# Optimization experiments

Measured on AMD Instinct MI355X. Metric: run time of the kernel, lower is better.

Reference implementation:

```python
import jax, jax.numpy as jnp
import numpy as np

BS, QLEN, DIM, NH = 2, 2048, 1024, 16
HD = DIM // NH


def setup_inputs() -> dict:
    key = jax.random.key(0)
    ks = jax.random.split(key, 6)
    std = 0.02
    return {
        "x": jax.random.normal(ks[0], (BS, QLEN, DIM), dtype=jnp.float32),
        "mask": jnp.ones((BS, QLEN), dtype=jnp.float32),
        "Wq": jax.random.normal(ks[1], (DIM, DIM), dtype=jnp.float32) * std,
        "bq": jnp.zeros((DIM,), dtype=jnp.float32),
        "Wk": jax.random.normal(ks[2], (DIM, DIM), dtype=jnp.float32) * std,
        "bk": jnp.zeros((DIM,), dtype=jnp.float32),
        "Wv": jax.random.normal(ks[3], (DIM, DIM), dtype=jnp.float32) * std,
        "bv": jnp.zeros((DIM,), dtype=jnp.float32),
        "Wo": jax.random.normal(ks[4], (DIM, DIM), dtype=jnp.float32) * std,
        "bo": jnp.zeros((DIM,), dtype=jnp.float32),
    }


def reference(x, mask, Wq, bq, Wk, bk, Wv, bv, Wo, bo):
    bs, qlen, dim = x.shape
    # project and split heads: [bs, nh, len, hd]
    def split_heads(t):
        return t.reshape(bs, -1, NH, HD).transpose(0, 2, 1, 3)

    q = split_heads(x @ Wq + bq) / jnp.sqrt(jnp.float32(HD))
    k = split_heads(x @ Wk + bk)
    v = split_heads(x @ Wv + bv)

    scores = jnp.einsum("bhqd,bhkd->bhqk", q, k)  # [bs, nh, qlen, klen]
    m = mask.reshape(bs, 1, 1, -1)  # 2D mask -> broadcast over heads and q
    scores = scores - 1e30 * (1.0 - m)
    weights = jax.nn.softmax(scores, axis=-1)
    # dropout p=0.0 at inference -> no-op; head_mask is None
    context = jnp.einsum("bhqk,bhkd->bhqd", weights, v)
    context = context.transpose(0, 2, 1, 3).reshape(bs, qlen, NH * HD)
    return context @ Wo + bo
```

## Files before the change

### kernel.cpp

```cpp
#include <hip/hip_runtime.h>
#include <stdint.h>

#define BSZ  2
#define SEQ  2048
#define DIM  1024
#define NHD  16
#define HD   64
#define MTOT (BSZ*SEQ)

using short8  = __attribute__((ext_vector_type(8))) short;
using floatx4 = __attribute__((ext_vector_type(4))) float;

#define QSCALE 0.18033688011112042f
#define BIGM   1.44e30f

__device__ __forceinline__ unsigned short f2bf(float f) {
    unsigned int u = __float_as_uint(f);
    u += 0x7fffu + ((u >> 16) & 1u);
    return (unsigned short)(u >> 16);
}
__device__ __forceinline__ unsigned int pk2r(float a, float b) {
    unsigned int ua = __float_as_uint(a) + 0x8000u;
    unsigned int ub = __float_as_uint(b) + 0x8000u;
    return __builtin_amdgcn_perm(ub, ua, 0x07060302);
}

__device__ __forceinline__ void gll16(const void* g, const void* lds) {
    unsigned int loff = (unsigned int)(unsigned long long)lds;
    __builtin_amdgcn_global_load_lds(
        (const __attribute__((address_space(1))) unsigned int*)g,
        (__attribute__((address_space(3))) unsigned int*)loff, 16, 0, 0);
}

__global__ __launch_bounds__(256)
void conv_x(const float* __restrict__ X, unsigned short* __restrict__ Xbf) {
    size_t i = ((size_t)blockIdx.x * 256 + threadIdx.x) * 8;
    float4 a = *(const float4*)(X + i);
    float4 b = *(const float4*)(X + i + 4);
    uint4 u = {pk2r(a.x, a.y), pk2r(a.z, a.w), pk2r(b.x, b.y), pk2r(b.z, b.w)};
    *(uint4*)(Xbf + i) = u;
}

__global__ __launch_bounds__(256)
void conv_wt(const float* __restrict__ Wq, const float* __restrict__ Wk,
             const float* __restrict__ Wv, const float* __restrict__ Wo,
             unsigned short* __restrict__ Wt3, unsigned short* __restrict__ Wto)
{
    __shared__ float tile[64 * 65];
    const int z = blockIdx.z;
    const float* W = (z == 0) ? Wq : (z == 1) ? Wk : (z == 2) ? Wv : Wo;
    unsigned short* out = (z < 3) ? (Wt3 + (size_t)z * DIM * DIM) : Wto;
    const int k0 = blockIdx.x * 64, n0 = blockIdx.y * 64;
    const int t = threadIdx.x;
    const int r = t >> 2, c0 = (t & 3) * 16;
#pragma unroll
    for (int j = 0; j < 4; ++j) {
        float4 v = *(const float4*)&W[(size_t)(k0 + r) * DIM + n0 + c0 + j * 4];
        tile[r * 65 + c0 + j * 4 + 0] = v.x;
        tile[r * 65 + c0 + j * 4 + 1] = v.y;
        tile[r * 65 + c0 + j * 4 + 2] = v.z;
        tile[r * 65 + c0 + j * 4 + 3] = v.w;
    }
    __syncthreads();
    unsigned int p[8];
#pragma unroll
    for (int j = 0; j < 8; ++j)
        p[j] = pk2r(tile[(c0 + 2 * j) * 65 + r], tile[(c0 + 2 * j + 1) * 65 + r]);
    uint4 u0 = {p[0], p[1], p[2], p[3]}, u1 = {p[4], p[5], p[6], p[7]};
    unsigned short* dst = out + (size_t)(n0 + r) * DIM + k0 + c0;
    *(uint4*)dst = u0;
    *(uint4*)(dst + 8) = u1;
}

__global__ __launch_bounds__(256)
void qkv_gemm(const unsigned short* __restrict__ Xbf,
              const unsigned short* __restrict__ Wt3,
              const float* __restrict__ bq, const float* __restrict__ bk,
              const float* __restrict__ bv,
              unsigned short* __restrict__ Qb,
              unsigned short* __restrict__ Kb,
              unsigned short* __restrict__ VbT)
{
    __shared__ unsigned short As[2][128 * 32];
    __shared__ unsigned short Bs[2][128 * 32];

    const int t = threadIdx.x, w = t >> 6, lane = t & 63;
    const int lm = lane & 15, grp = lane >> 4;
    const int wm = w >> 1, wn = w & 1;
    const int m0 = blockIdx.x * 128;
    const int mat = blockIdx.y >> 3;
    const int n0 = (blockIdx.y & 7) * 128;
    const unsigned short* Bg = Wt3 + (size_t)mat * DIM * DIM;
    const int lr = lane >> 2, lc = (lane & 3) * 8;
    const int r0 = w * 16;
    const bool swap = (mat != 2);

    const unsigned short* xs0 = Xbf + (size_t)(m0 + r0 + lr) * DIM + lc;
    const unsigned short* xs1 = Xbf + (size_t)(m0 + 64 + r0 + lr) * DIM + lc;
    const unsigned short* ws0 = Bg  + (size_t)(n0 + r0 + lr) * DIM + lc;
    const unsigned short* ws1 = Bg  + (size_t)(n0 + 64 + r0 + lr) * DIM + lc;

    const unsigned short* afb[2];
    const unsigned short* bfb[2];
#pragma unroll
    for (int u = 0; u < 2; ++u) {
        afb[u] = &As[u][(wm * 64 + lm) * 32 + grp * 8];
        bfb[u] = &Bs[u][(wn * 64 + lm) * 32 + grp * 8];
    }

    floatx4 acc[4][4];
#pragma unroll
    for (int i = 0; i < 4; ++i)
#pragma unroll
        for (int j = 0; j < 4; ++j) acc[i][j] = (floatx4){0.f, 0.f, 0.f, 0.f};

#define QKV_STAGE(BUF) do {                                    \
        gll16(xs0, &As[BUF][r0 * 32]);                         \
        gll16(xs1, &As[BUF][(64 + r0) * 32]);                  \
        gll16(ws0, &Bs[BUF][r0 * 32]);                         \
        gll16(ws1, &Bs[BUF][(64 + r0) * 32]);                  \
        xs0 += 32; xs1 += 32; ws0 += 32; ws1 += 32;            \
    } while (0)

#define QKV_BODY(CUR) do {                                                    \
        __syncthreads();                                                      \
        QKV_STAGE(CUR ^ 1);                                                   \
        short8 af[4], bf[4];                                                  \
        _Pragma("unroll")                                                     \
        for (int mt = 0; mt < 4; ++mt)                                        \
            af[mt] = *(const short8*)(afb[CUR] + mt * 512);                   \
        _Pragma("unroll")                                                     \
        for (int nt = 0; nt < 4; ++nt)                                        \
            bf[nt] = *(const short8*)(bfb[CUR] + nt * 512);                   \
        if (swap) {                                                           \
            _Pragma("unroll")                                                 \
            for (int mt = 0; mt < 4; ++mt)                                    \
                _Pragma("unroll")                                             \
                for (int nt = 0; nt < 4; ++nt)                                \
                    acc[mt][nt] = __builtin_amdgcn_mfma_f32_16x16x32_bf16(    \
                        bf[nt], af[mt], acc[mt][nt], 0, 0, 0);                \
        } else {                                                              \
            _Pragma("unroll")                                                 \
            for (int mt = 0; mt < 4; ++mt)                                    \
                _Pragma("unroll")                                             \
                for (int nt = 0; nt < 4; ++nt)                                \
                    acc[mt][nt] = __builtin_amdgcn_mfma_f32_16x16x32_bf16(    \
                        af[mt], bf[nt], acc[mt][nt], 0, 0, 0);                \
        }                                                                     \
    } while (0)

    QKV_STAGE(0);
#pragma unroll 1
    for (int it = 0; it < DIM / 64; ++it) {
        QKV_BODY(0);
        QKV_BODY(1);
    }
#undef QKV_BODY
#undef QKV_STAGE

    if (mat == 2) {
#pragma unroll
        for (int nt = 0; nt < 4; ++nt) {
            const int c = n0 + wn * 64 + nt * 16 + lm;
            const float bb = bv[c];
            const int h = c >> 6, d = c & 63;
#pragma unroll
            for (int mt = 0; mt < 4; ++mt) {
                const int r = m0 + wm * 64 + mt * 16 + grp * 4;
                const int b = r >> 11, s = r & 2047;
                const int si = s & 63, sb = s & ~63;
                const int cg = si >> 4, g = (si >> 2) & 3;
                const int unit = (((cg & 1) << 2) | g) ^ (d & 7);
                const int sph = sb + unit * 8 + ((cg >> 1) << 2);
                uint2 pv;
                pv.x = pk2r(acc[mt][nt][0] + bb, acc[mt][nt][1] + bb);
                pv.y = pk2r(acc[mt][nt][2] + bb, acc[mt][nt][3] + bb);
                *(uint2*)&VbT[(((size_t)(b * NHD + h)) * HD + d) * SEQ + sph] = pv;
            }
        }
    } else {
        const float* bias = (mat == 0) ? bq : bk;
        unsigned short* dst = (mat == 0) ? Qb : Kb;
        const float sc = (mat == 0) ? QSCALE : 1.0f;
#pragma unroll
        for (int nt = 0; nt < 4; ++nt) {
            const int c0 = n0 + wn * 64 + nt * 16 + grp * 4;
            float4 bb = *(const float4*)&bias[c0];
            const int h = c0 >> 6, d0 = c0 & 63;
#pragma unroll
            for (int mt = 0; mt < 4; ++mt) {
                const int r = m0 + wm * 64 + mt * 16 + lm;
                const int b = r >> 11, s = r & 2047;
                uint2 pv;
                pv.x = pk2r((acc[mt][nt][0] + bb.x) * sc, (acc[mt][nt][1] + bb.y) * sc);
                pv.y = pk2r((acc[mt][nt][2] + bb.z) * sc, (acc[mt][nt][3] + bb.w) * sc);
                const int dd = (mat == 0) ? d0
                             : ((((d0 >> 3) ^ (s & 7)) << 3) | (d0 & 7));
                *(uint2*)&dst[(((size_t)(b * NHD + h)) * SEQ + s) * HD + dd] = pv;
            }
        }
    }
}

__global__ __launch_bounds__(256, 4)
void attn(const unsigned short* __restrict__ Qb,
          const unsigned short* __restrict__ Kb,
          const unsigned short* __restrict__ VbT,
          const float* __restrict__ mask,
          unsigned short* __restrict__ Cb)
{
    __shared__ unsigned short Kt[2][64 * 64];
    __shared__ unsigned short Vt[2][64 * 64];
    __shared__ float Msk[SEQ];

    const int t = threadIdx.x, w = t >> 6, lane = t & 63;
    const int lm = lane & 15, grp = lane >> 4;
    const int x7 = lm & 7;
    const int bh = blockIdx.y, b = bh >> 4, h = bh & 15;
    const int q0 = blockIdx.x * 64;

    short8 qf[2];
    {
        const unsigned short* qrow = Qb + ((size_t)bh * SEQ + q0 + w * 16 + lm) * HD;
        qf[0] = *(const short8*)(qrow + grp * 8);
        qf[1] = *(const short8*)(qrow + 32 + grp * 8);
    }

    {
        const float* mb = mask + b * SEQ;
        const int i = t * 8;
        float4 a = *(const float4*)(mb + i);
        float4 c = *(const float4*)(mb + i + 4);
        float4 ra = {__builtin_fmaf(a.x, BIGM, -BIGM), __builtin_fmaf(a.y, BIGM, -BIGM),
                     __builtin_fmaf(a.z, BIGM, -BIGM), __builtin_fmaf(a.w, BIGM, -BIGM)};
        float4 rc = {__builtin_fmaf(c.x, BIGM, -BIGM), __builtin_fmaf(c.y, BIGM, -BIGM),
                     __builtin_fmaf(c.z, BIGM, -BIGM), __builtin_fmaf(c.w, BIGM, -BIGM)};
        *(float4*)&Msk[i]     = ra;
        *(float4*)&Msk[i + 4] = rc;
    }

    floatx4 oacc[4];
#pragma unroll
    for (int i = 0; i < 4; ++i) oacc[i] = (floatx4){0.f, 0.f, 0.f, 0.f};
    float lpart = 0.f;

    const unsigned short* Kg = Kb + (size_t)bh * SEQ * HD;
    const unsigned short* Vg = VbT + (size_t)bh * HD * SEQ;
    const int srow = lane >> 3, scol = (lane & 7) * 8;

    const unsigned short* kp0 = Kg + (size_t)(w * 16 + srow) * HD + scol;
    const unsigned short* kp1 = kp0 + 8 * HD;
    const unsigned short* vp0 = Vg + (size_t)(w * 16 + srow) * SEQ + scol;
    const unsigned short* vp1 = vp0 + 8 * SEQ;

    gll16(kp0, &Kt[0][(w * 16) * 64]);
    gll16(kp1, &Kt[0][(w * 16 + 8) * 64]);
    gll16(vp0, &Vt[0][(w * 16) * 64]);
    gll16(vp1, &Vt[0][(w * 16 + 8) * 64]);
    kp0 += 64 * HD; kp1 += 64 * HD; vp0 += 64; vp1 += 64;

    const unsigned short* kba[2]; const unsigned short* kbb[2];
    const unsigned short* vba[2]; const unsigned short* vbb[2];
#pragma unroll
    for (int u = 0; u < 2; ++u) {
        kba[u] = &Kt[u][lm * 64 + ((grp    ) ^ x7) * 8];
        kbb[u] = &Kt[u][lm * 64 + ((4 + grp) ^ x7) * 8];
        vba[u] = &Vt[u][lm * 64 + ((grp    ) ^ x7) * 8];
        vbb[u] = &Vt[u][lm * 64 + ((4 + grp) ^ x7) * 8];
    }
    const float* mp = &Msk[grp * 4];

#define ATTN_BODY(CUR) do {                                                   \
        __syncthreads();                                                      \
        gll16(kp0, &Kt[CUR ^ 1][(w * 16) * 64]);                              \
        gll16(kp1, &Kt[CUR ^ 1][(w * 16 + 8) * 64]);                          \
        gll16(vp0, &Vt[CUR ^ 1][(w * 16) * 64]);                              \
        gll16(vp1, &Vt[CUR ^ 1][(w * 16 + 8) * 64]);                          \
        kp0 += 64 * HD; kp1 += 64 * HD; vp0 += 64; vp1 += 64;                 \
        floatx4 sv[4];                                                        \
        _Pragma("unroll")                                                     \
        for (int cg = 0; cg < 4; ++cg) {                                      \
            short8 a0 = *(const short8*)(kba[CUR] + cg * 1024);               \
            short8 a1 = *(const short8*)(kbb[CUR] + cg * 1024);               \
            floatx4 s = (floatx4){0.f, 0.f, 0.f, 0.f};                        \
            s = __builtin_amdgcn_mfma_f32_16x16x32_bf16(a0, qf[0], s, 0, 0, 0); \
            s = __builtin_amdgcn_mfma_f32_16x16x32_bf16(a1, qf[1], s, 0, 0, 0); \
            sv[cg] = s;                                                       \
        }                                                                     \
        short8 vf[4][2];                                                      \
        _Pragma("unroll")                                                     \
        for (int dg = 0; dg < 4; ++dg) {                                      \
            vf[dg][0] = *(const short8*)(vba[CUR] + dg * 1024);               \
            vf[dg][1] = *(const short8*)(vbb[CUR] + dg * 1024);               \
        }                                                                     \
        float p[4][4];                                                        \
        _Pragma("unroll")                                                     \
        for (int cg = 0; cg < 4; ++cg) {                                      \
            float4 md = *(const float4*)(mp + cg * 16);                       \
            p[cg][0] = __builtin_exp2f(sv[cg][0] + md.x);                     \
            p[cg][1] = __builtin_exp2f(sv[cg][1] + md.y);                     \
            p[cg][2] = __builtin_exp2f(sv[cg][2] + md.z);                     \
            p[cg][3] = __builtin_exp2f(sv[cg][3] + md.w);                     \
            lpart += (p[cg][0] + p[cg][1]) + (p[cg][2] + p[cg][3]);           \
        }                                                                     \
        mp += 64;                                                             \
        uint4 u0, u1;                                                         \
        u0.x = pk2r(p[0][0], p[0][1]); u0.y = pk2r(p[0][2], p[0][3]);         \
        u0.z = pk2r(p[2][0], p[2][1]); u0.w = pk2r(p[2][2], p[2][3]);         \
        u1.x = pk2r(p[1][0], p[1][1]); u1.y = pk2r(p[1][2], p[1][3]);         \
        u1.z = pk2r(p[3][0], p[3][1]); u1.w = pk2r(p[3][2], p[3][3]);         \
        short8 ap0 = *(const short8*)&u0;                                     \
        short8 ap1 = *(const short8*)&u1;                                     \
        _Pragma("unroll")                                                     \
        for (int dg = 0; dg < 4; ++dg) {                                      \
            oacc[dg] = __builtin_amdgcn_mfma_f32_16x16x32_bf16(ap0, vf[dg][0], oacc[dg], 0, 0, 0); \
            oacc[dg] = __builtin_amdgcn_mfma_f32_16x16x32_bf16(ap1, vf[dg][1], oacc[dg], 0, 0, 0); \
        }                                                                     \
    } while (0)

#pragma unroll 1
    for (int it = 0; it < SEQ / 128; ++it) {
        ATTN_BODY(0);
        ATTN_BODY(1);
    }
#undef ATTN_BODY

    lpart += __shfl_xor(lpart, 16);
    lpart += __shfl_xor(lpart, 32);
    const float linv = (lpart > 0.f) ? 1.0f / lpart : 0.f;
    float inv[4];
#pragma unroll
    for (int r = 0; r < 4; ++r) inv[r] = __shfl(linv, grp * 4 + r);
#pragma unroll
    for (int dg = 0; dg < 4; ++dg)
#pragma unroll
        for (int r = 0; r < 4; ++r) {
            const int s = q0 + w * 16 + grp * 4 + r;
            Cb[((size_t)(b * SEQ + s)) * DIM + h * HD + dg * 16 + lm] =
                f2bf(oacc[dg][r] * inv[r]);
        }
}

__global__ __launch_bounds__(256)
void out_gemm(const unsigned short* __restrict__ Cb,
              const unsigned short* __restrict__ Wto,
              const float* __restrict__ bo,
              float* __restrict__ out)
{
    __shared__ unsigned short As[2][128 * 32];
    __shared__ unsigned short Bs[2][64 * 32];

    const int t = threadIdx.x, w = t >> 6, lane = t & 63;
    const int lm = lane & 15, grp = lane >> 4;
    const int m0 = blockIdx.x * 128;
    const int n0 = blockIdx.y * 64;
    const int lr = lane >> 2, lc = (lane & 3) * 8;
    const int r0 = w * 16;

    const unsigned short* cs0 = Cb  + (size_t)(m0 + r0 + lr) * DIM + lc;
    const unsigned short* cs1 = Cb  + (size_t)(m0 + 64 + r0 + lr) * DIM + lc;
    const unsigned short* ws0 = Wto + (size_t)(n0 + r0 + lr) * DIM + lc;

    const unsigned short* afb[2];
    const unsigned short* bfb[2];
#pragma unroll
    for (int u = 0; u < 2; ++u) {
        afb[u] = &As[u][(w * 32 + lm) * 32 + grp * 8];
        bfb[u] = &Bs[u][lm * 32 + grp * 8];
    }

    floatx4 acc[2][4];
#pragma unroll
    for (int i = 0; i < 2; ++i)
#pragma unroll
        for (int j = 0; j < 4; ++j) acc[i][j] = (floatx4){0.f, 0.f, 0.f, 0.f};

#define OUT_STAGE(BUF) do {                                    \
        gll16(cs0, &As[BUF][r0 * 32]);                         \
        gll16(cs1, &As[BUF][(64 + r0) * 32]);                  \
        gll16(ws0, &Bs[BUF][r0 * 32]);                         \
        cs0 += 32; cs1 += 32; ws0 += 32;                       \
    } while (0)

#define OUT_BODY(CUR) do {                                                    \
        __syncthreads();                                                      \
        OUT_STAGE(CUR ^ 1);                                                   \
        short8 af[2], bf[4];                                                  \
        _Pragma("unroll")                                                     \
        for (int mt = 0; mt < 2; ++mt)                                        \
            af[mt] = *(const short8*)(afb[CUR] + mt * 512);                   \
        _Pragma("unroll")                                                     \
        for (int nt = 0; nt < 4; ++nt)                                        \
            bf[nt] = *(const short8*)(bfb[CUR] + nt * 512);                   \
        _Pragma("unroll")                                                     \
        for (int mt = 0; mt < 2; ++mt)                                        \
            _Pragma("unroll")                                                 \
            for (int nt = 0; nt < 4; ++nt)                                    \
                acc[mt][nt] = __builtin_amdgcn_mfma_f32_16x16x32_bf16(        \
                    bf[nt], af[mt], acc[mt][nt], 0, 0, 0);                    \
    } while (0)

    OUT_STAGE(0);
#pragma unroll 1
    for (int it = 0; it < DIM / 64; ++it) {
        OUT_BODY(0);
        OUT_BODY(1);
    }
#undef OUT_BODY
#undef OUT_STAGE

#pragma unroll
    for (int nt = 0; nt < 4; ++nt) {
        const int c0 = n0 + nt * 16 + grp * 4;
        float4 bb = *(const float4*)&bo[c0];
#pragma unroll
        for (int mt = 0; mt < 2; ++mt) {
            const int r = m0 + w * 32 + mt * 16 + lm;
            float4 o = {acc[mt][nt][0] + bb.x, acc[mt][nt][1] + bb.y,
                        acc[mt][nt][2] + bb.z, acc[mt][nt][3] + bb.w};
            *(float4*)&out[(size_t)r * DIM + c0] = o;
        }
    }
}

extern "C" void kernel_launch(void* const* d_in, const int* in_sizes, int n_in,
                              void* d_out, int out_size, void* d_ws, size_t ws_size,
                              hipStream_t stream)
{
    const float* x    = (const float*)d_in[0];
    const float* mask = (const float*)d_in[1];
    const float* Wq   = (const float*)d_in[2];
    const float* bq   = (const float*)d_in[3];
    const float* Wk   = (const float*)d_in[4];
    const float* bk   = (const float*)d_in[5];
    const float* Wv   = (const float*)d_in[6];
    const float* bv   = (const float*)d_in[7];
    const float* Wo   = (const float*)d_in[8];
    const float* bo   = (const float*)d_in[9];
    float* out = (float*)d_out;

    const size_t M1 = (size_t)DIM * DIM;
    unsigned short* Qb  = (unsigned short*)d_ws;
    unsigned short* Kb  = Qb  + 4 * M1;
    unsigned short* VbT = Kb  + 4 * M1;
    unsigned short* Cb  = VbT + 4 * M1;
    unsigned short* Xbf = Cb  + 4 * M1;
    unsigned short* Wt3 = Xbf + 4 * M1;
    unsigned short* Wto = Wt3 + 3 * M1;

    conv_x <<<dim3((MTOT * DIM) / 2048), 256, 0, stream>>>(x, Xbf);
    conv_wt<<<dim3(16, 16, 4), 256, 0, stream>>>(Wq, Wk, Wv, Wo, Wt3, Wto);
    qkv_gemm<<<dim3(MTOT / 128, 24), 256, 0, stream>>>(Xbf, Wt3, bq, bk, bv, Qb, Kb, VbT);
    attn<<<dim3(SEQ / 64, BSZ * NHD), 256, 0, stream>>>(Qb, Kb, VbT, mask, Cb);
    out_gemm<<<dim3(MTOT / 128, DIM / 64), 256, 0, stream>>>(Cb, Wto, bo, out);
}
```

Before: 208.6 us.

## Precompute mask penalty globally, fold into MFMA init, swizzle attn blocks, use cvt_pk_bf16

Mask-penalty computation moves from each attention block's LDS prologue into conv_x, which writes a global penalty array. The attention loop reads that array directly and uses it as the initial MFMA accumulator, so the separate add before exp2 goes away. The change also remaps block indices so neighbouring blocks fall on different heads, and replaces the manual rounding bf16 pack with the hardware v_cvt_pk_bf16_f32 instruction. In exchange, each iteration now does global (cache-resident) mask loads instead of LDS reads, and the workspace needs extra space for the penalty array.

```diff
diff --git a/kernel.cpp b/kernel.cpp
--- a/kernel.cpp
+++ b/kernel.cpp
@@ -24,6 +24,11 @@
     unsigned int ub = __float_as_uint(b) + 0x8000u;
     return __builtin_amdgcn_perm(ub, ua, 0x07060302);
 }
+__device__ __forceinline__ unsigned int cvtpk(float a, float b) {
+    unsigned int r;
+    asm("v_cvt_pk_bf16_f32 %0, %1, %2" : "=v"(r) : "v"(a), "v"(b));
+    return r;
+}
 
 __device__ __forceinline__ void gll16(const void* g, const void* lds) {
     unsigned int loff = (unsigned int)(unsigned long long)lds;
@@ -33,12 +38,24 @@
 }
 
 __global__ __launch_bounds__(256)
-void conv_x(const float* __restrict__ X, unsigned short* __restrict__ Xbf) {
+void conv_x(const float* __restrict__ X, const float* __restrict__ mask,
+            unsigned short* __restrict__ Xbf, float* __restrict__ Pen) {
     size_t i = ((size_t)blockIdx.x * 256 + threadIdx.x) * 8;
     float4 a = *(const float4*)(X + i);
     float4 b = *(const float4*)(X + i + 4);
     uint4 u = {pk2r(a.x, a.y), pk2r(a.z, a.w), pk2r(b.x, b.y), pk2r(b.z, b.w)};
     *(uint4*)(Xbf + i) = u;
+    if (blockIdx.x < 2) {
+        const size_t j = ((size_t)blockIdx.x * 256 + threadIdx.x) * 8;
+        float4 m0 = *(const float4*)(mask + j);
+        float4 m1 = *(const float4*)(mask + j + 4);
+        float4 r0 = {__builtin_fmaf(m0.x, BIGM, -BIGM), __builtin_fmaf(m0.y, BIGM, -BIGM),
+                     __builtin_fmaf(m0.z, BIGM, -BIGM), __builtin_fmaf(m0.w, BIGM, -BIGM)};
+        float4 r1 = {__builtin_fmaf(m1.x, BIGM, -BIGM), __builtin_fmaf(m1.y, BIGM, -BIGM),
+                     __builtin_fmaf(m1.z, BIGM, -BIGM), __builtin_fmaf(m1.w, BIGM, -BIGM)};
+        *(float4*)(Pen + j)     = r0;
+        *(float4*)(Pen + j + 4) = r1;
+    }
 }
 
 __global__ __launch_bounds__(256)
@@ -206,18 +223,20 @@
 void attn(const unsigned short* __restrict__ Qb,
           const unsigned short* __restrict__ Kb,
           const unsigned short* __restrict__ VbT,
-          const float* __restrict__ mask,
+          const float* __restrict__ Pen,
           unsigned short* __restrict__ Cb)
 {
     __shared__ unsigned short Kt[2][64 * 64];
     __shared__ unsigned short Vt[2][64 * 64];
-    __shared__ float Msk[SEQ];
 
     const int t = threadIdx.x, w = t >> 6, lane = t & 63;
     const int lm = lane & 15, grp = lane >> 4;
     const int x7 = lm & 7;
-    const int bh = blockIdx.y, b = bh >> 4, h = bh & 15;
-    const int q0 = blockIdx.x * 64;
+
+    const int lin = blockIdx.y * (int)gridDim.x + blockIdx.x;
+    const int swz = (lin & 7) * ((SEQ / 64) * (BSZ * NHD) / 8) + (lin >> 3);
+    const int bh = swz >> 5, b = bh >> 4, h = bh & 15;
+    const int q0 = (swz & 31) * 64;
 
     short8 qf[2];
     {
@@ -226,19 +245,6 @@
         qf[1] = *(const short8*)(qrow + 32 + grp * 8);
     }
 
-    {
-        const float* mb = mask + b * SEQ;
-        const int i = t * 8;
-        float4 a = *(const float4*)(mb + i);
-        float4 c = *(const float4*)(mb + i + 4);
-        float4 ra = {__builtin_fmaf(a.x, BIGM, -BIGM), __builtin_fmaf(a.y, BIGM, -BIGM),
-                     __builtin_fmaf(a.z, BIGM, -BIGM), __builtin_fmaf(a.w, BIGM, -BIGM)};
-        float4 rc = {__builtin_fmaf(c.x, BIGM, -BIGM), __builtin_fmaf(c.y, BIGM, -BIGM),
-                     __builtin_fmaf(c.z, BIGM, -BIGM), __builtin_fmaf(c.w, BIGM, -BIGM)};
-        *(float4*)&Msk[i]     = ra;
-        *(float4*)&Msk[i + 4] = rc;
-    }
-
     floatx4 oacc[4];
 #pragma unroll
     for (int i = 0; i < 4; ++i) oacc[i] = (floatx4){0.f, 0.f, 0.f, 0.f};
@@ -268,7 +274,7 @@
         vba[u] = &Vt[u][lm * 64 + ((grp    ) ^ x7) * 8];
         vbb[u] = &Vt[u][lm * 64 + ((4 + grp) ^ x7) * 8];
     }
-    const float* mp = &Msk[grp * 4];
+    const float* mp = Pen + (size_t)b * SEQ + grp * 4;
 
 #define ATTN_BODY(CUR) do {                                                   \
         __syncthreads();                                                      \
@@ -277,12 +283,17 @@
         gll16(vp0, &Vt[CUR ^ 1][(w * 16) * 64]);                              \
         gll16(vp1, &Vt[CUR ^ 1][(w * 16 + 8) * 64]);                          \
         kp0 += 64 * HD; kp1 += 64 * HD; vp0 += 64; vp1 += 64;                 \
+        float4 mdv[4];                                                        \
+        _Pragma("unroll")                                                     \
+        for (int cg = 0; cg < 4; ++cg)                                        \
+            mdv[cg] = *(const float4*)(mp + cg * 16);                         \
+        mp += 64;                                                             \
         floatx4 sv[4];                                                        \
         _Pragma("unroll")                                                     \
         for (int cg = 0; cg < 4; ++cg) {                                      \
             short8 a0 = *(const short8*)(kba[CUR] + cg * 1024);               \
             short8 a1 = *(const short8*)(kbb[CUR] + cg * 1024);               \
-            floatx4 s = (floatx4){0.f, 0.f, 0.f, 0.f};                        \
+            floatx4 s = (floatx4){mdv[cg].x, mdv[cg].y, mdv[cg].z, mdv[cg].w}; \
             s = __builtin_amdgcn_mfma_f32_16x16x32_bf16(a0, qf[0], s, 0, 0, 0); \
             s = __builtin_amdgcn_mfma_f32_16x16x32_bf16(a1, qf[1], s, 0, 0, 0); \
             sv[cg] = s;                                                       \
@@ -296,19 +307,17 @@
         float p[4][4];                                                        \
         _Pragma("unroll")                                                     \
         for (int cg = 0; cg < 4; ++cg) {                                      \
-            float4 md = *(const float4*)(mp + cg * 16);                       \
-            p[cg][0] = __builtin_exp2f(sv[cg][0] + md.x);                     \
-            p[cg][1] = __builtin_exp2f(sv[cg][1] + md.y);                     \
-            p[cg][2] = __builtin_exp2f(sv[cg][2] + md.z);                     \
-            p[cg][3] = __builtin_exp2f(sv[cg][3] + md.w);                     \
+            p[cg][0] = __builtin_exp2f(sv[cg][0]);                            \
+            p[cg][1] = __builtin_exp2f(sv[cg][1]);                            \
+            p[cg][2] = __builtin_exp2f(sv[cg][2]);                            \
+            p[cg][3] = __builtin_exp2f(sv[cg][3]);                            \
             lpart += (p[cg][0] + p[cg][1]) + (p[cg][2] + p[cg][3]);           \
         }                                                                     \
-        mp += 64;                                                             \
         uint4 u0, u1;                                                         \
-        u0.x = pk2r(p[0][0], p[0][1]); u0.y = pk2r(p[0][2], p[0][3]);         \
-        u0.z = pk2r(p[2][0], p[2][1]); u0.w = pk2r(p[2][2], p[2][3]);         \
-        u1.x = pk2r(p[1][0], p[1][1]); u1.y = pk2r(p[1][2], p[1][3]);         \
-        u1.z = pk2r(p[3][0], p[3][1]); u1.w = pk2r(p[3][2], p[3][3]);         \
+        u0.x = cvtpk(p[0][0], p[0][1]); u0.y = cvtpk(p[0][2], p[0][3]);       \
+        u0.z = cvtpk(p[2][0], p[2][1]); u0.w = cvtpk(p[2][2], p[2][3]);       \
+        u1.x = cvtpk(p[1][0], p[1][1]); u1.y = cvtpk(p[1][2], p[1][3]);       \
+        u1.z = cvtpk(p[3][0], p[3][1]); u1.w = cvtpk(p[3][2], p[3][3]);       \
         short8 ap0 = *(const short8*)&u0;                                     \
         short8 ap1 = *(const short8*)&u1;                                     \
         _Pragma("unroll")                                                     \
@@ -447,10 +456,11 @@
     unsigned short* Xbf = Cb  + 4 * M1;
     unsigned short* Wt3 = Xbf + 4 * M1;
     unsigned short* Wto = Wt3 + 3 * M1;
-
-    conv_x <<<dim3((MTOT * DIM) / 2048), 256, 0, stream>>>(x, Xbf);
+    float*          Pen = (float*)(Wto + M1);
+
+    conv_x <<<dim3((MTOT * DIM) / 2048), 256, 0, stream>>>(x, mask, Xbf, Pen);
     conv_wt<<<dim3(16, 16, 4), 256, 0, stream>>>(Wq, Wk, Wv, Wo, Wt3, Wto);
     qkv_gemm<<<dim3(MTOT / 128, 24), 256, 0, stream>>>(Xbf, Wt3, bq, bk, bv, Qb, Kb, VbT);
-    attn<<<dim3(SEQ / 64, BSZ * NHD), 256, 0, stream>>>(Qb, Kb, VbT, mask, Cb);
+    attn<<<dim3(SEQ / 64, BSZ * NHD), 256, 0, stream>>>(Qb, Kb, VbT, Pen, Cb);
     out_gemm<<<dim3(MTOT / 128, DIM / 64), 256, 0, stream>>>(Cb, Wto, bo, out);
 }
```

After: 204.9 us. Within noise of the previous version (-1.8%).
